# Performance work log

Hardware: AMD Instinct MI355X
Metric: run time of the kernel (lower is better)

## Reference

```python
import jax, jax.numpy as jnp
import numpy as np

B, H, W, C = 4, 128, 128, 192
NH, WS, SS = 6, 16, 8
N = WS * WS
HD = C // NH
SCALE = HD ** -0.5
CONV_SCALE = 0.01


def _win_part(x, ws):
    b, h, w, c = x.shape
    x = x.reshape(b, h // ws, ws, w // ws, ws, c).transpose(0, 1, 3, 2, 4, 5)
    return x.reshape(-1, ws * ws, c)


def _win_rev(win, ws, h, w):
    b = win.shape[0] // ((h // ws) * (w // ws))
    x = win.reshape(b, h // ws, w // ws, ws, ws, -1).transpose(0, 1, 3, 2, 4, 5)
    return x.reshape(b, h, w, -1)


def _ln(x, g, b):
    m = x.mean(-1, keepdims=True)
    v = x.var(-1, keepdims=True)
    return (x - m) * jax.lax.rsqrt(v + 1e-5) * g + b


def _conv3(x, w, b):
    return jax.lax.conv_general_dilated(x, w, (1, 1), 'SAME', dimension_numbers=('NHWC', 'HWIO', 'NHWC')) + b


def _rpi_sa(ws):
    coords = np.stack(np.meshgrid(np.arange(ws), np.arange(ws), indexing='ij'))
    cf = coords.reshape(2, -1)
    rc = (cf[:, :, None] - cf[:, None, :]).transpose(1, 2, 0).copy()
    rc[:, :, 0] += ws - 1
    rc[:, :, 1] += ws - 1
    rc[:, :, 0] *= 2 * ws - 1
    return rc.sum(-1)


def _attn_mask(h, w, ws, ss):
    img = np.zeros((1, h, w, 1), dtype=np.float32)
    slices = (slice(0, -ws), slice(-ws, -ss), slice(-ss, None))
    cnt = 0
    for hs in slices:
        for wsl in slices:
            img[:, hs, wsl, :] = cnt
            cnt += 1
    mw = img.reshape(1, h // ws, ws, w // ws, ws, 1).transpose(0, 1, 3, 2, 4, 5).reshape(-1, ws * ws)
    am = mw[:, None, :] - mw[:, :, None]
    return np.where(am != 0, -100.0, 0.0).astype(np.float32)


def setup_inputs() -> dict:
    key = jax.random.key(0)
    ks = jax.random.split(key, 10)
    std = 0.02
    return {
        'x': jax.random.normal(ks[0], (B, H * W, C), jnp.float32),
        'qkv_w': jax.random.normal(ks[1], (C, 3 * C), jnp.float32) * std,
        'qkv_b': jnp.zeros((3 * C,), jnp.float32),
        'proj_w': jax.random.normal(ks[2], (C, C), jnp.float32) * std,
        'proj_b': jnp.zeros((C,), jnp.float32),
        'rpb': jax.random.normal(ks[3], ((2 * WS - 1) ** 2, NH), jnp.float32) * std,
        'norm1_w': jnp.ones((C,), jnp.float32),
        'norm1_b': jnp.zeros((C,), jnp.float32),
        'norm2_w': jnp.ones((C,), jnp.float32),
        'norm2_b': jnp.zeros((C,), jnp.float32),
        'conv1_w': jax.random.normal(ks[4], (3, 3, C, C // 3), jnp.float32) * std,
        'conv1_b': jnp.zeros((C // 3,), jnp.float32),
        'conv2_w': jax.random.normal(ks[5], (3, 3, C // 3, C), jnp.float32) * std,
        'conv2_b': jnp.zeros((C,), jnp.float32),
        'ca1_w': jax.random.normal(ks[6], (C, C // 30), jnp.float32) * std,
        'ca1_b': jnp.zeros((C // 30,), jnp.float32),
        'ca2_w': jax.random.normal(ks[7], (C // 30, C), jnp.float32) * std,
        'ca2_b': jnp.zeros((C,), jnp.float32),
        'fc1_w': jax.random.normal(ks[8], (C, 4 * C), jnp.float32) * std,
        'fc1_b': jnp.zeros((4 * C,), jnp.float32),
        'fc2_w': jax.random.normal(ks[9], (4 * C, C), jnp.float32) * std,
        'fc2_b': jnp.zeros((C,), jnp.float32),
        'rpi': jnp.asarray(_rpi_sa(WS), jnp.int32),
        'attn_mask': jnp.asarray(_attn_mask(H, W, WS, SS)),
    }


def reference(x, qkv_w, qkv_b, proj_w, proj_b, rpb, norm1_w, norm1_b, norm2_w, norm2_b,
              conv1_w, conv1_b, conv2_w, conv2_b, ca1_w, ca1_b, ca2_w, ca2_b,
              fc1_w, fc1_b, fc2_w, fc2_b, rpi, attn_mask):
    b = x.shape[0]
    shortcut = x
    xn = _ln(x, norm1_w, norm1_b).reshape(b, H, W, C)

    # CAB conv branch: conv3x3 -> GELU -> conv3x3 -> channel attention
    cv = jax.nn.gelu(_conv3(xn, conv1_w, conv1_b), approximate=False)
    cv = _conv3(cv, conv2_w, conv2_b)
    pooled = cv.mean(axis=(1, 2))                                  # [b, C] global avg pool
    ca = jax.nn.sigmoid(jnp.maximum(pooled @ ca1_w + ca1_b, 0.0) @ ca2_w + ca2_b)
    conv_x = (cv * ca[:, None, None, :]).reshape(b, H * W, C)

    # shifted window attention
    shifted = jnp.roll(xn, (-SS, -SS), axis=(1, 2))
    xw = _win_part(shifted, WS)                                    # [b*nw, N, C]
    b_ = xw.shape[0]
    qkv = (xw @ qkv_w + qkv_b).reshape(b_, N, 3, NH, HD).transpose(2, 0, 3, 1, 4)
    q, k, v = qkv[0] * SCALE, qkv[1], qkv[2]                       # [b_, NH, N, HD]
    attn = jnp.einsum('whnd,whmd->whnm', q, k)                     # [b_, NH, N, N]
    bias = rpb[rpi.reshape(-1)].reshape(N, N, NH).transpose(2, 0, 1)
    attn = attn + bias[None]
    nw = attn_mask.shape[0]
    attn = attn.reshape(b, nw, NH, N, N) + attn_mask[None, :, None]
    attn = jax.nn.softmax(attn, axis=-1).reshape(b_, NH, N, N)
    out = jnp.einsum('whnm,whmd->whnd', attn, v).transpose(0, 2, 1, 3).reshape(b_, N, C)
    out = out @ proj_w + proj_b
    rev = _win_rev(out, WS, H, W)
    attn_x = jnp.roll(rev, (SS, SS), axis=(1, 2)).reshape(b, H * W, C)

    y = shortcut + attn_x + conv_x * CONV_SCALE

    # MLP
    yn = _ln(y, norm2_w, norm2_b)
    mlp = jax.nn.gelu(yn @ fc1_w + fc1_b, approximate=False) @ fc2_w + fc2_b
    return y + mlp
```

## Files before the change

kernel.cpp:

```cpp
#include <hip/hip_runtime.h>
#include <hip/hip_bf16.h>
#include <cstdint>
#include <cstddef>

#define BB 4
#define CC 192
#define NHEAD 6
#define WSZ 16
#define SSH 8
#define NTOK 256
#define HD 32
#define HWPIX 16384
#define TTOT 65536
#define WWID 128
#define SCALE_Q 0.17677669529663687f
#define CONV_SC 0.01f
#define PSTR 264
#define KSTR 40

typedef __hip_bfloat16 bf16;
typedef __attribute__((ext_vector_type(8))) short short8;
typedef __attribute__((ext_vector_type(4))) float float4v;

__device__ __forceinline__ float b2f(bf16 v) { return __bfloat162float(v); }
__device__ __forceinline__ bf16 f2b(float v) { return __float2bfloat16(v); }
__device__ __forceinline__ unsigned short f2bu(float f) {
  bf16 h = __float2bfloat16(f);
  return *reinterpret_cast<unsigned short*>(&h);
}
__device__ __forceinline__ float gelu_exact(float x) {
  return 0.5f * x * (1.0f + erff(x * 0.7071067811865475f));
}
__device__ __forceinline__ short8 ld8z(const bf16* p, bool ok) {
  if (ok) return *(const short8*)p;
  short8 z = {0, 0, 0, 0, 0, 0, 0, 0};
  return z;
}
__device__ __forceinline__ void glds16(const void* g, void* l) {
  __builtin_amdgcn_global_load_lds(
      (const __attribute__((address_space(1))) unsigned int*)g,
      (__attribute__((address_space(3))) unsigned int*)l, 16, 0, 0);
}

__global__ __launch_bounds__(256) void k_ln1(const float* __restrict__ x,
                                             const float* __restrict__ g,
                                             const float* __restrict__ b,
                                             bf16* __restrict__ xn) {
  int wv = threadIdx.x >> 6, lane = threadIdx.x & 63;
  int tok = blockIdx.x * 4 + wv;
  size_t row = (size_t)tok * CC;
  float v0 = x[row + lane], v1 = x[row + lane + 64], v2 = x[row + lane + 128];
  float s = v0 + v1 + v2, ss = v0 * v0 + v1 * v1 + v2 * v2;
#pragma unroll
  for (int off = 1; off < 64; off <<= 1) {
    s += __shfl_xor(s, off, 64);
    ss += __shfl_xor(ss, off, 64);
  }
  float mean = s * (1.0f / CC);
  float rstd = rsqrtf(ss * (1.0f / CC) - mean * mean + 1e-5f);
  xn[row + lane]       = f2b((v0 - mean) * rstd * g[lane]       + b[lane]);
  xn[row + lane + 64]  = f2b((v1 - mean) * rstd * g[lane + 64]  + b[lane + 64]);
  xn[row + lane + 128] = f2b((v2 - mean) * rstd * g[lane + 128] + b[lane + 128]);
}

__global__ __launch_bounds__(256) void k_biasq(const int* __restrict__ rpi,
                                               const float* __restrict__ rpb,
                                               float* __restrict__ biasQ) {
  int k = threadIdx.x;
  int h = blockIdx.x >> 8;
  int q = blockIdx.x & 255;
  biasQ[(size_t)blockIdx.x * 256 + ((k & 15) << 4) + (k >> 4)] =
      rpb[rpi[q * 256 + k] * NHEAD + h];
}

__global__ __launch_bounds__(256) void k_wprep(const float* __restrict__ c1w,
                                               const float* __restrict__ c2w,
                                               bf16* __restrict__ wT1,
                                               bf16* __restrict__ wT2) {
  int i = blockIdx.x * 256 + threadIdx.x;
  {
    int tap = i / (64 * 192); int r = i % (64 * 192);
    int oc = r / 192, ci = r % 192;
    wT1[i] = f2b(c1w[(size_t)(tap * 192 + ci) * 64 + oc]);
  }
  {
    int tap = i / (192 * 64); int r = i % (192 * 64);
    int oc = r / 64, ci = r % 64;
    wT2[i] = f2b(c2w[(size_t)(tap * 64 + ci) * 192 + oc]);
  }
}

__global__ __launch_bounds__(256) void k_wprep2(const float* __restrict__ fc1w,
                                                const float* __restrict__ fc2w,
                                                bf16* __restrict__ wF1,
                                                bf16* __restrict__ wF2) {
  int i = blockIdx.x * 256 + threadIdx.x;
  {
    int n = i / 192, k = i % 192;
    wF1[i] = f2b(fc1w[(size_t)k * 768 + n]);
  }
  {
    int n = i / 768, k = i % 768;
    wF2[i] = f2b(fc2w[(size_t)k * 192 + n]);
  }
}

__global__ __launch_bounds__(256) void k_wprep3(const float* __restrict__ qkvw,
                                                const float* __restrict__ projw,
                                                bf16* __restrict__ wQv,
                                                bf16* __restrict__ wP) {
  int i = blockIdx.x * 256 + threadIdx.x;
  if (i < 576 * 192) {
    int n = i / 192, k = i % 192;
    wQv[i] = f2b(qkvw[(size_t)k * 576 + n]);
  }
  if (i < 192 * 192) {
    int n = i / 192, k = i % 192;
    wP[i] = f2b(projw[(size_t)k * 192 + n]);
  }
}

__global__ __launch_bounds__(256, 2) void k_qkvws(const bf16* __restrict__ xn,
                                                  const bf16* __restrict__ wQv,
                                                  const float* __restrict__ qb,
                                                  bf16* __restrict__ Qg,
                                                  bf16* __restrict__ Kg,
                                                  bf16* __restrict__ Vg) {
  __shared__ unsigned short wl[192 * 192];
  int cg = blockIdx.x / 128, tb = blockIdx.x - cg * 128;
  int tid = threadIdx.x;
  int wave = tid >> 6, lane = tid & 63;
  int lm = lane & 15, lq = lane >> 4;

  const char* src = (const char*)wQv + (size_t)cg * 73728;
#pragma unroll
  for (int j = 0; j < 18; ++j) {
    int ci = j * 256 + tid;
    int r = ci / 24, c = ci - r * 24;
    glds16(src + (size_t)r * 384 + ((c ^ (r & 7)) << 4),
           (char*)wl + (size_t)(j * 256 + wave * 64) * 16);
  }
  __syncthreads();

  short8 wfr[3][6];
#pragma unroll
  for (int nt = 0; nt < 3; ++nt) {
    int rl = wave * 48 + nt * 16 + lm;
#pragma unroll
    for (int ks = 0; ks < 6; ++ks)
      wfr[nt][ks] = *(const short8*)&wl[rl * 192 + (((ks * 4 + lq) ^ (rl & 7)) << 3)];
  }
  float4 b4[3];
  int head[3], d0[3];
#pragma unroll
  for (int nt = 0; nt < 3; ++nt) {
    int n0p = wave * 48 + nt * 16 + lq * 4;
    b4[nt] = *(const float4*)(qb + cg * 192 + n0p);
    head[nt] = n0p >> 5;
    d0[nt] = n0p & 31;
  }
  bf16* dst = (cg == 0) ? Qg : (cg == 1) ? Kg : Vg;
  float scale = (cg == 0) ? SCALE_Q : 1.f;

  int tok0b = tb * 512;
#pragma unroll 2
  for (int t = 0; t < 32; ++t) {
    int tok0 = tok0b + t * 16;
    const bf16* arow = xn + (size_t)(tok0 + lm) * CC + lq * 8;
    int tg = tok0 + lm;
    int b = tg >> 14;
    int pix = tg & 16383;
    int gh = pix >> 7, gw = pix & 127;
    int hs = (gh + 120) & 127, wsx = (gw + 120) & 127;
    int wdx = (b << 6) + ((hs >> 4) << 3) + (wsx >> 4);
    int ndx = ((hs & 15) << 4) + (wsx & 15);
    size_t base = ((size_t)wdx * NHEAD) * NTOK * HD + (size_t)ndx * HD;

    float4v acc[3];
#pragma unroll
    for (int nt = 0; nt < 3; ++nt) acc[nt] = (float4v){0.f, 0.f, 0.f, 0.f};
#pragma unroll
    for (int ks = 0; ks < 6; ++ks) {
      short8 tf = *(const short8*)(arow + ks * 32);
#pragma unroll
      for (int nt = 0; nt < 3; ++nt)
        acc[nt] = __builtin_amdgcn_mfma_f32_16x16x32_bf16(wfr[nt][ks], tf, acc[nt], 0, 0, 0);
    }
#pragma unroll
    for (int nt = 0; nt < 3; ++nt) {
      unsigned short u0 = f2bu((acc[nt][0] + b4[nt].x) * scale);
      unsigned short u1 = f2bu((acc[nt][1] + b4[nt].y) * scale);
      unsigned short u2 = f2bu((acc[nt][2] + b4[nt].z) * scale);
      unsigned short u3 = f2bu((acc[nt][3] + b4[nt].w) * scale);
      uint2 pk;
      pk.x = (unsigned)u0 | ((unsigned)u1 << 16);
      pk.y = (unsigned)u2 | ((unsigned)u3 << 16);
      *(uint2*)(dst + base + (size_t)head[nt] * NTOK * HD + d0[nt]) = pk;
    }
  }
}

__global__ __launch_bounds__(256) void k_attn3(const bf16* __restrict__ Qg,
                                               const bf16* __restrict__ Kg,
                                               const bf16* __restrict__ Vg,
                                               const float* __restrict__ biasP,
                                               bf16* __restrict__ AO) {
  __shared__ unsigned short PTw[4][16 * PSTR];
  __shared__ unsigned short VT[32 * PSTR];
  __shared__ unsigned short KL[256 * KSTR];
  int wh = blockIdx.x >> 1, half = blockIdx.x & 1;
  int wdx = wh / NHEAD, h = wh - wdx * NHEAD;
  int wl = wdx & 63;
  int wr = wl >> 3, wc = wl & 7;
  int tid = threadIdx.x;
  int wave = tid >> 6, lane = tid & 63;
  int lm = lane & 15, lq = lane >> 4;
  int q0 = half * 128;
  bool needmask = (wr == 7) || (wc == 7);

  {
    const uint4* vp = (const uint4*)(Vg + ((size_t)wh * NTOK + tid) * HD);
    uint4 vv[4] = {vp[0], vp[1], vp[2], vp[3]};
    const uint4* kp = (const uint4*)(Kg + ((size_t)wh * NTOK + tid) * HD);
    uint4 kv[4] = {kp[0], kp[1], kp[2], kp[3]};
#pragma unroll
    for (int i = 0; i < 4; ++i) {
      unsigned arr[4] = {vv[i].x, vv[i].y, vv[i].z, vv[i].w};
#pragma unroll
      for (int j = 0; j < 4; ++j) {
        int d = i * 8 + j * 2;
        VT[d * PSTR + tid]       = (unsigned short)(arr[j] & 0xffffu);
        VT[(d + 1) * PSTR + tid] = (unsigned short)(arr[j] >> 16);
      }
      *(uint4*)&KL[tid * KSTR + i * 8] = kv[i];
    }
  }
  __syncthreads();

  int wsk = (wc << 4) + lm;
  int ridk_w = (wsk >= 112) + (wsk >= 120);
  unsigned short* PT = &PTw[wave][0];

  float4v oacc[2][2];
#pragma unroll
  for (int rt = 0; rt < 2; ++rt)
#pragma unroll
    for (int c2 = 0; c2 < 2; ++c2) oacc[rt][c2] = (float4v){0.f, 0.f, 0.f, 0.f};
  float linv[2][4];

#pragma unroll
  for (int rt = 0; rt < 2; ++rt) {
    int qrow = q0 + wave * 32 + rt * 16;
    short8 aq = *(const short8*)(Qg + ((size_t)wh * NTOK + qrow + lm) * HD + lq * 8);
    float4v sacc[16];
#pragma unroll
    for (int ct = 0; ct < 16; ++ct) sacc[ct] = (float4v){0.f, 0.f, 0.f, 0.f};
#pragma unroll
    for (int ct = 0; ct < 16; ++ct) {
      short8 kf = *(const short8*)&KL[(ct * 16 + lm) * KSTR + lq * 8];
      sacc[ct] = __builtin_amdgcn_mfma_f32_16x16x32_bf16(aq, kf, sacc[ct], 0, 0, 0);
    }
#pragma unroll
    for (int reg = 0; reg < 4; ++reg) {
      int nq = qrow + lq * 4 + reg;
      const float* bp = biasP + ((size_t)(h * 256 + nq)) * 256 + lm * 16;
      float bb[16];
      *(float4*)&bb[0]  = ((const float4*)bp)[0];
      *(float4*)&bb[4]  = ((const float4*)bp)[1];
      *(float4*)&bb[8]  = ((const float4*)bp)[2];
      *(float4*)&bb[12] = ((const float4*)bp)[3];
      float sv[16];
      float mx = -1.0e30f;
      if (needmask) {
        int hsq = (wr << 4) + (nq >> 4), wsq = (wc << 4) + (nq & 15);
        int ridq = ((hsq >= 112) + (hsq >= 120)) * 3 + ((wsq >= 112) + (wsq >= 120));
#pragma unroll
        for (int ct = 0; ct < 16; ++ct) {
          int hsk = (wr << 4) + ct;
          int ridk = ((hsk >= 112) + (hsk >= 120)) * 3 + ridk_w;
          float s = sacc[ct][reg] + bb[ct] + ((ridk != ridq) ? -100.f : 0.f);
          sv[ct] = s;
          mx = fmaxf(mx, s);
        }
      } else {
#pragma unroll
        for (int ct = 0; ct < 16; ++ct) {
          float s = sacc[ct][reg] + bb[ct];
          sv[ct] = s;
          mx = fmaxf(mx, s);
        }
      }
#pragma unroll
      for (int off = 1; off < 16; off <<= 1) mx = fmaxf(mx, __shfl_xor(mx, off, 64));
      float l = 0.f;
#pragma unroll
      for (int ct = 0; ct < 16; ++ct) {
        float p = __expf(sv[ct] - mx);
        l += p;
        PT[(lq * 4 + reg) * PSTR + ct * 16 + lm] = f2bu(p);
      }
#pragma unroll
      for (int off = 1; off < 16; off <<= 1) l += __shfl_xor(l, off, 64);
      linv[rt][reg] = 1.f / l;
    }
#pragma unroll
    for (int kb = 0; kb < 8; ++kb) {
      short8 pf = *(const short8*)&PT[lm * PSTR + kb * 32 + lq * 8];
#pragma unroll
      for (int c2 = 0; c2 < 2; ++c2) {
        short8 vf = *(const short8*)&VT[(c2 * 16 + lm) * PSTR + kb * 32 + lq * 8];
        oacc[rt][c2] = __builtin_amdgcn_mfma_f32_16x16x32_bf16(pf, vf, oacc[rt][c2], 0, 0, 0);
      }
    }
  }
#pragma unroll
  for (int rt = 0; rt < 2; ++rt)
#pragma unroll
    for (int c2 = 0; c2 < 2; ++c2) {
      int d = c2 * 16 + lm;
#pragma unroll
      for (int reg = 0; reg < 4; ++reg) {
        int nq = q0 + wave * 32 + rt * 16 + lq * 4 + reg;
        AO[((size_t)wdx * NTOK + nq) * CC + h * HD + d] =
            f2b(oacc[rt][c2][reg] * linv[rt][reg]);
      }
    }
}

__global__ __launch_bounds__(256, 2) void k_projws(const bf16* __restrict__ AO,
                                                   const bf16* __restrict__ wP,
                                                   const float* __restrict__ pb,
                                                   const float* __restrict__ x,
                                                   float* __restrict__ y) {
  __shared__ unsigned short wl[192 * 192];
  int tb = blockIdx.x;
  int tid = threadIdx.x;
  int wave = tid >> 6, lane = tid & 63;
  int lm = lane & 15, lq = lane >> 4;

  const char* src = (const char*)wP;
#pragma unroll
  for (int j = 0; j < 18; ++j) {
    int ci = j * 256 + tid;
    int r = ci / 24, c = ci - r * 24;
    glds16(src + (size_t)r * 384 + ((c ^ (r & 7)) << 4),
           (char*)wl + (size_t)(j * 256 + wave * 64) * 16);
  }
  __syncthreads();

  short8 wfr[3][6];
#pragma unroll
  for (int nt = 0; nt < 3; ++nt) {
    int rl = wave * 48 + nt * 16 + lm;
#pragma unroll
    for (int ks = 0; ks < 6; ++ks)
      wfr[nt][ks] = *(const short8*)&wl[rl * 192 + (((ks * 4 + lq) ^ (rl & 7)) << 3)];
  }
  float4 b4[3];
#pragma unroll
  for (int nt = 0; nt < 3; ++nt)
    b4[nt] = *(const float4*)(pb + wave * 48 + nt * 16 + lq * 4);

  int r0b = tb * 512;
#pragma unroll 2
  for (int t = 0; t < 32; ++t) {
    int r0 = r0b + t * 16;
    const bf16* arow = AO + (size_t)(r0 + lm) * CC + lq * 8;
    int r = r0 + lm;
    int wdx = r >> 8, n = r & 255;
    int wb = wdx >> 6, wlx = wdx & 63;
    int hs = ((wlx >> 3) << 4) + (n >> 4);
    int wsx = ((wlx & 7) << 4) + (n & 15);
    int gh = (hs + SSH) & 127, gw = (wsx + SSH) & 127;
    size_t drow = ((size_t)wb * HWPIX + (size_t)gh * WWID + gw) * CC;

    float4v acc[3];
#pragma unroll
    for (int nt = 0; nt < 3; ++nt) acc[nt] = (float4v){0.f, 0.f, 0.f, 0.f};
#pragma unroll
    for (int ks = 0; ks < 6; ++ks) {
      short8 tf = *(const short8*)(arow + ks * 32);
#pragma unroll
      for (int nt = 0; nt < 3; ++nt)
        acc[nt] = __builtin_amdgcn_mfma_f32_16x16x32_bf16(wfr[nt][ks], tf, acc[nt], 0, 0, 0);
    }
#pragma unroll
    for (int nt = 0; nt < 3; ++nt) {
      int col0 = wave * 48 + nt * 16 + lq * 4;
      float4 xv = *(const float4*)(x + drow + col0);
      float4 ov;
      ov.x = xv.x + acc[nt][0] + b4[nt].x;
      ov.y = xv.y + acc[nt][1] + b4[nt].y;
      ov.z = xv.z + acc[nt][2] + b4[nt].z;
      ov.w = xv.w + acc[nt][3] + b4[nt].w;
      *(float4*)(y + drow + col0) = ov;
    }
  }
}

__global__ __launch_bounds__(512, 1) void k_conv1l(const bf16* __restrict__ xn,
                                                   const bf16* __restrict__ wT1,
                                                   const float* __restrict__ c1b,
                                                   bf16* __restrict__ cv1) {
  __shared__ unsigned short xs[3 * 128 * 192];
  int hh = blockIdx.x & 127, b = blockIdx.x >> 7;
  int tid = threadIdx.x;
  int wave = tid >> 6, lane = tid & 63;
  int lm = lane & 15, lq = lane >> 4;
  int ph = wave >> 2;
  int oc = (wave & 3) * 16 + lm;

#pragma unroll
  for (int r = 0; r < 3; ++r) {
    int gh = hh + r - 1;
    if ((unsigned)gh < 128u) {
      const char* src = (const char*)(xn + (size_t)(b * HWPIX + gh * WWID) * CC);
#pragma unroll
      for (int j = 0; j < 6; ++j) {
        int c = j * 512 + tid;
        int px = c / 24, kc = c - px * 24;
        glds16(src + (size_t)px * 384 + ((size_t)(kc ^ (px & 7)) << 4),
               (char*)xs + ((size_t)(r * 3072 + j * 512 + wave * 64)) * 16);
      }
    }
  }
  __syncthreads();

  float4v acc[4];
#pragma unroll
  for (int t = 0; t < 4; ++t) acc[t] = (float4v){0.f, 0.f, 0.f, 0.f};

  short8 w[6], wn[6];
#pragma unroll
  for (int ks = 0; ks < 6; ++ks)
    w[ks] = *(const short8*)(wT1 + ((size_t)oc) * CC + ks * 32 + lq * 8);
#pragma unroll
  for (int tap = 0; tap < 9; ++tap) {
    if (tap < 8) {
#pragma unroll
      for (int ks = 0; ks < 6; ++ks)
        wn[ks] = *(const short8*)(wT1 + ((size_t)((tap + 1) * 64) + oc) * CC + ks * 32 + lq * 8);
    }
    int kh = tap / 3, kw = tap % 3;
    int gh = hh + kh - 1;
    if ((unsigned)gh < 128u) {
      const unsigned short* row = &xs[kh * 24576];
#pragma unroll
      for (int ks = 0; ks < 6; ++ks) {
#pragma unroll
        for (int t = 0; t < 4; ++t) {
          int px = ph * 64 + t * 16 + lm + kw - 1;
          int pxc = px < 0 ? 0 : (px > 127 ? 127 : px);
          short8 av = *(const short8*)&row[pxc * 192 + (((ks * 4 + lq) ^ (pxc & 7)) << 3)];
          short8 zz = {0, 0, 0, 0, 0, 0, 0, 0};
          short8 a = ((unsigned)px < 128u) ? av : zz;
          acc[t] = __builtin_amdgcn_mfma_f32_16x16x32_bf16(a, w[ks], acc[t], 0, 0, 0);
        }
      }
    }
#pragma unroll
    for (int ks = 0; ks < 6; ++ks) w[ks] = wn[ks];
  }
  float bias = c1b[oc];
#pragma unroll
  for (int t = 0; t < 4; ++t) {
    int pxb = ph * 64 + t * 16 + lq * 4;
    size_t base = ((size_t)b * HWPIX + (size_t)hh * WWID + pxb) * 64 + oc;
    cv1[base]       = f2b(gelu_exact(acc[t][0] + bias));
    cv1[base + 64]  = f2b(gelu_exact(acc[t][1] + bias));
    cv1[base + 128] = f2b(gelu_exact(acc[t][2] + bias));
    cv1[base + 192] = f2b(gelu_exact(acc[t][3] + bias));
  }
}

__global__ __launch_bounds__(512, 2) void k_conv2l(const bf16* __restrict__ cv1,
                                                   const bf16* __restrict__ wT2,
                                                   const float* __restrict__ c2b,
                                                   bf16* __restrict__ cv2) {
  __shared__ unsigned short cs[3 * 128 * 64];
  int hh = blockIdx.x & 127, b = blockIdx.x >> 7;
  int tid = threadIdx.x;
  int wave = tid >> 6, lane = tid & 63;
  int lm = lane & 15, lq = lane >> 4;
  int ph = wave >> 2;
  int og = wave & 3;

#pragma unroll
  for (int r = 0; r < 3; ++r) {
    int gh = hh + r - 1;
    if ((unsigned)gh < 128u) {
      const char* src = (const char*)(cv1 + (size_t)(b * HWPIX + gh * WWID) * 64);
#pragma unroll
      for (int j = 0; j < 2; ++j) {
        int c = j * 512 + tid;
        int px = c >> 3, kc = c & 7;
        glds16(src + (size_t)px * 128 + ((size_t)(kc ^ (px & 7)) << 4),
               (char*)cs + ((size_t)(r * 1024 + j * 512 + wave * 64)) * 16);
      }
    }
  }
  __syncthreads();

  float4v acc[3][4];
#pragma unroll
  for (int nt = 0; nt < 3; ++nt)
#pragma unroll
    for (int t = 0; t < 4; ++t) acc[nt][t] = (float4v){0.f, 0.f, 0.f, 0.f};

  short8 w[3][2], wn[3][2];
#pragma unroll
  for (int nt = 0; nt < 3; ++nt) {
    int oc = og * 48 + nt * 16 + lm;
#pragma unroll
    for (int ks = 0; ks < 2; ++ks)
      w[nt][ks] = *(const short8*)(wT2 + ((size_t)oc) * 64 + ks * 32 + lq * 8);
  }
#pragma unroll
  for (int tap = 0; tap < 9; ++tap) {
    if (tap < 8) {
#pragma unroll
      for (int nt = 0; nt < 3; ++nt) {
        int oc = og * 48 + nt * 16 + lm;
#pragma unroll
        for (int ks = 0; ks < 2; ++ks)
          wn[nt][ks] = *(const short8*)(wT2 + ((size_t)((tap + 1) * 192) + oc) * 64 + ks * 32 + lq * 8);
      }
    }
    int kh = tap / 3, kw = tap % 3;
    int gh = hh + kh - 1;
    if ((unsigned)gh < 128u) {
      const unsigned short* row = &cs[kh * 8192];
#pragma unroll
      for (int ks = 0; ks < 2; ++ks) {
#pragma unroll
        for (int t = 0; t < 4; ++t) {
          int px = ph * 64 + t * 16 + lm + kw - 1;
          int pxc = px < 0 ? 0 : (px > 127 ? 127 : px);
          short8 av = *(const short8*)&row[pxc * 64 + (((ks * 4 + lq) ^ (pxc & 7)) << 3)];
          short8 zz = {0, 0, 0, 0, 0, 0, 0, 0};
          short8 a = ((unsigned)px < 128u) ? av : zz;
#pragma unroll
          for (int nt = 0; nt < 3; ++nt)
            acc[nt][t] = __builtin_amdgcn_mfma_f32_16x16x32_bf16(a, w[nt][ks], acc[nt][t], 0, 0, 0);
        }
      }
    }
#pragma unroll
    for (int nt = 0; nt < 3; ++nt)
#pragma unroll
      for (int ks = 0; ks < 2; ++ks) w[nt][ks] = wn[nt][ks];
  }
#pragma unroll
  for (int nt = 0; nt < 3; ++nt) {
    int oc = og * 48 + nt * 16 + lm;
    float bias = c2b[oc];
#pragma unroll
    for (int t = 0; t < 4; ++t) {
      int pxb = ph * 64 + t * 16 + lq * 4;
      size_t base = ((size_t)b * HWPIX + (size_t)hh * WWID + pxb) * CC + oc;
      cv2[base]           = f2b(acc[nt][t][0] + bias);
      cv2[base + CC]      = f2b(acc[nt][t][1] + bias);
      cv2[base + 2 * CC]  = f2b(acc[nt][t][2] + bias);
      cv2[base + 3 * CC]  = f2b(acc[nt][t][3] + bias);
    }
  }
}

__global__ __launch_bounds__(192) void k_pool(const bf16* __restrict__ cv2,
                                              float* __restrict__ pooled) {
  int t = threadIdx.x;
  int b = blockIdx.x >> 7;
  int pc = blockIdx.x & 127;
  const bf16* base = cv2 + ((size_t)b * HWPIX + (size_t)pc * 128) * CC + t;
  float s = 0.f;
#pragma unroll 4
  for (int p = 0; p < 128; ++p) s += b2f(base[(size_t)p * CC]);
  atomicAdd(&pooled[b * CC + t], s);
}

__global__ __launch_bounds__(192) void k_ca(const float* __restrict__ pooled,
                                            const float* __restrict__ w1,
                                            const float* __restrict__ b1,
                                            const float* __restrict__ w2,
                                            const float* __restrict__ b2,
                                            float* __restrict__ ca) {
  __shared__ float pld[CC];
  __shared__ float t1[6];
  int t = threadIdx.x, b = blockIdx.x;
  pld[t] = pooled[b * CC + t] * (1.0f / HWPIX);
  __syncthreads();
  if (t < 6) {
    float s = b1[t];
    for (int c = 0; c < CC; ++c) s += pld[c] * w1[c * 6 + t];
    t1[t] = fmaxf(s, 0.f);
  }
  __syncthreads();
  float s = b2[t];
#pragma unroll
  for (int k = 0; k < 6; ++k) s += t1[k] * w2[k * CC + t];
  ca[b * CC + t] = 1.f / (1.f + __expf(-s));
}

__global__ __launch_bounds__(256) void k_ln2(const float* __restrict__ y,
                                             const bf16* __restrict__ cv2,
                                             const float* __restrict__ ca,
                                             const float* __restrict__ g2,
                                             const float* __restrict__ b2,
                                             bf16* __restrict__ yn) {
  int wv = threadIdx.x >> 6, lane = threadIdx.x & 63;
  int tok = blockIdx.x * 4 + wv;
  const float* cab = ca + (tok >> 14) * CC;
  size_t row = (size_t)tok * CC;
  float v0 = y[row + lane]       + b2f(cv2[row + lane])       * cab[lane]       * CONV_SC;
  float v1 = y[row + lane + 64]  + b2f(cv2[row + lane + 64])  * cab[lane + 64]  * CONV_SC;
  float v2 = y[row + lane + 128] + b2f(cv2[row + lane + 128]) * cab[lane + 128] * CONV_SC;
  float s = v0 + v1 + v2, ss = v0 * v0 + v1 * v1 + v2 * v2;
#pragma unroll
  for (int off = 1; off < 64; off <<= 1) {
    s += __shfl_xor(s, off, 64);
    ss += __shfl_xor(ss, off, 64);
  }
  float mean = s * (1.0f / CC);
  float rstd = rsqrtf(ss * (1.0f / CC) - mean * mean + 1e-5f);
  yn[row + lane]       = f2b((v0 - mean) * rstd * g2[lane]       + b2[lane]);
  yn[row + lane + 64]  = f2b((v1 - mean) * rstd * g2[lane + 64]  + b2[lane + 64]);
  yn[row + lane + 128] = f2b((v2 - mean) * rstd * g2[lane + 128] + b2[lane + 128]);
}

__global__ __launch_bounds__(256, 2) void k_fc1ws(const bf16* __restrict__ yn,
                                                  const bf16* __restrict__ wF1,
                                                  const float* __restrict__ fb1,
                                                  bf16* __restrict__ h) {
  __shared__ unsigned short wl[192 * 192];
  int cg = blockIdx.x & 3, tb = blockIdx.x >> 2;
  int tid = threadIdx.x;
  int wave = tid >> 6, lane = tid & 63;
  int lm = lane & 15, lq = lane >> 4;

  const char* src = (const char*)wF1 + (size_t)cg * 73728;
#pragma unroll
  for (int j = 0; j < 18; ++j) {
    int ci = j * 256 + tid;
    int r = ci / 24, c = ci - r * 24;
    glds16(src + (size_t)r * 384 + ((c ^ (r & 7)) << 4),
           (char*)wl + (size_t)(j * 256 + wave * 64) * 16);
  }
  __syncthreads();

  short8 wfr[3][6];
#pragma unroll
  for (int nt = 0; nt < 3; ++nt) {
    int rl = wave * 48 + nt * 16 + lm;
#pragma unroll
    for (int ks = 0; ks < 6; ++ks)
      wfr[nt][ks] = *(const short8*)&wl[rl * 192 + (((ks * 4 + lq) ^ (rl & 7)) << 3)];
  }
  float4 b4[3];
#pragma unroll
  for (int nt = 0; nt < 3; ++nt)
    b4[nt] = *(const float4*)(fb1 + cg * 192 + wave * 48 + nt * 16 + lq * 4);

  int tok0b = tb * 512;
#pragma unroll 2
  for (int t = 0; t < 32; ++t) {
    int tok0 = tok0b + t * 16;
    const bf16* arow = yn + (size_t)(tok0 + lm) * CC + lq * 8;
    float4v acc[3];
#pragma unroll
    for (int nt = 0; nt < 3; ++nt) acc[nt] = (float4v){0.f, 0.f, 0.f, 0.f};
#pragma unroll
    for (int ks = 0; ks < 6; ++ks) {
      short8 tf = *(const short8*)(arow + ks * 32);
#pragma unroll
      for (int nt = 0; nt < 3; ++nt)
        acc[nt] = __builtin_amdgcn_mfma_f32_16x16x32_bf16(wfr[nt][ks], tf, acc[nt], 0, 0, 0);
    }
    bf16* hrow = h + (size_t)(tok0 + lm) * 768 + cg * 192 + wave * 48 + lq * 4;
#pragma unroll
    for (int nt = 0; nt < 3; ++nt) {
      unsigned short u0 = f2bu(gelu_exact(acc[nt][0] + b4[nt].x));
      unsigned short u1 = f2bu(gelu_exact(acc[nt][1] + b4[nt].y));
      unsigned short u2 = f2bu(gelu_exact(acc[nt][2] + b4[nt].z));
      unsigned short u3 = f2bu(gelu_exact(acc[nt][3] + b4[nt].w));
      uint2 pk;
      pk.x = (unsigned)u0 | ((unsigned)u1 << 16);
      pk.y = (unsigned)u2 | ((unsigned)u3 << 16);
      *(uint2*)(hrow + nt * 16) = pk;
    }
  }
}

__global__ __launch_bounds__(256, 2) void k_fc2m(const bf16* __restrict__ h,
                                                 const bf16* __restrict__ wF2,
                                                 const float* __restrict__ fb2,
                                                 const float* __restrict__ y,
                                                 const bf16* __restrict__ cv2,
                                                 const float* __restrict__ ca,
                                                 float* __restrict__ out) {
  __shared__ unsigned short ha[2][4096];
  __shared__ unsigned short wbt[2][6144];
  int r0 = blockIdx.x * 128;
  int tid = threadIdx.x;
  int wave = tid >> 6, lane = tid & 63;
  int lm = lane & 15, lq = lane >> 4;

  const char* hsrc = (const char*)(h + (size_t)r0 * 768);
  const char* wsrc = (const char*)wF2;

  float4v acc[2][12];
#pragma unroll
  for (int mt = 0; mt < 2; ++mt)
#pragma unroll
    for (int nt = 0; nt < 12; ++nt) acc[mt][nt] = (float4v){0.f, 0.f, 0.f, 0.f};

  auto stage = [&](int kc, int b) {
    int k0b = kc * 64;
#pragma unroll
    for (int j = 0; j < 2; ++j) {
      int c = j * 256 + tid;
      glds16(hsrc + (size_t)(c >> 2) * 1536 + k0b + (c & 3) * 16,
             (char*)&ha[b][0] + (j * 256 + wave * 64) * 16);
    }
#pragma unroll
    for (int j = 0; j < 3; ++j) {
      int c = j * 256 + tid;
      glds16(wsrc + (size_t)(c >> 2) * 1536 + k0b + (c & 3) * 16,
             (char*)&wbt[b][0] + (j * 256 + wave * 64) * 16);
    }
  };

  stage(0, 0);
  __syncthreads();
#pragma unroll 1
  for (int kc = 0; kc < 24; ++kc) {
    int cur = kc & 1;
    if (kc < 23) stage(kc + 1, cur ^ 1);
    short8 af[2], bf[12];
#pragma unroll
    for (int mt = 0; mt < 2; ++mt)
      af[mt] = *(const short8*)&ha[cur][(wave * 32 + mt * 16 + lm) * 32 + lq * 8];
#pragma unroll
    for (int nt = 0; nt < 12; ++nt)
      bf[nt] = *(const short8*)&wbt[cur][(nt * 16 + lm) * 32 + lq * 8];
#pragma unroll
    for (int mt = 0; mt < 2; ++mt)
#pragma unroll
      for (int nt = 0; nt < 12; ++nt)
        acc[mt][nt] = __builtin_amdgcn_mfma_f32_16x16x32_bf16(af[mt], bf[nt], acc[mt][nt], 0, 0, 0);
    __syncthreads();
  }

  const float* cab = ca + (r0 >> 14) * CC;
#pragma unroll
  for (int nt = 0; nt < 12; ++nt) {
    int col = nt * 16 + lm;
    float bias = fb2[col];
    float cas = cab[col] * CONV_SC;
#pragma unroll
    for (int mt = 0; mt < 2; ++mt) {
#pragma unroll
      for (int reg = 0; reg < 4; ++reg) {
        int tok = r0 + wave * 32 + mt * 16 + lq * 4 + reg;
        size_t idx = (size_t)tok * CC + col;
        out[idx] = y[idx] + b2f(cv2[idx]) * cas + acc[mt][nt][reg] + bias;
      }
    }
  }
}

extern "C" void kernel_launch(void* const* d_in, const int* in_sizes, int n_in,
                              void* d_out, int out_size, void* d_ws, size_t ws_size,
                              hipStream_t stream) {
  const float* x      = (const float*)d_in[0];
  const float* qkv_w  = (const float*)d_in[1];
  const float* qkv_b  = (const float*)d_in[2];
  const float* proj_w = (const float*)d_in[3];
  const float* proj_b = (const float*)d_in[4];
  const float* rpb    = (const float*)d_in[5];
  const float* n1w    = (const float*)d_in[6];
  const float* n1b    = (const float*)d_in[7];
  const float* n2w    = (const float*)d_in[8];
  const float* n2b    = (const float*)d_in[9];
  const float* c1w    = (const float*)d_in[10];
  const float* c1b    = (const float*)d_in[11];
  const float* c2w    = (const float*)d_in[12];
  const float* c2b    = (const float*)d_in[13];
  const float* ca1w   = (const float*)d_in[14];
  const float* ca1b   = (const float*)d_in[15];
  const float* ca2w   = (const float*)d_in[16];
  const float* ca2b   = (const float*)d_in[17];
  const float* fc1w   = (const float*)d_in[18];
  const float* fc1b   = (const float*)d_in[19];
  const float* fc2w   = (const float*)d_in[20];
  const float* fc2b   = (const float*)d_in[21];
  const int*   rpi    = (const int*)d_in[22];
  (void)in_sizes; (void)n_in; (void)out_size; (void)ws_size;

  char* wsb = (char*)d_ws;
  bf16*  xn    = (bf16*)(wsb + 0);
  bf16*  yn    = (bf16*)(wsb + 0);
  float* biasQ = (float*)(wsb + 25165824);
  bf16*  Qg    = (bf16*)(wsb + 26738688);
  bf16*  Kg    = (bf16*)(wsb + 51904512);
  bf16*  Vg    = (bf16*)(wsb + 77070336);
  bf16*  AO    = (bf16*)(wsb + 102236160);
  bf16*  hbuf  = (bf16*)(wsb + 26738688);
  float* y     = (float*)(wsb + 127401984);
  bf16*  cv1   = (bf16*)(wsb + 177733632);
  bf16*  cv2   = (bf16*)(wsb + 186122240);
  float* pool  = (float*)(wsb + 211288064);
  float* cavec = (float*)(wsb + 211291136);
  bf16*  wT1   = (bf16*)(wsb + 211294208);
  bf16*  wT2   = (bf16*)(wsb + 211515392);
  bf16*  wF1   = (bf16*)(wsb + 211736576);
  bf16*  wF2   = (bf16*)(wsb + 212031488);
  bf16*  wQv   = (bf16*)(wsb + 212326400);
  bf16*  wP    = (bf16*)(wsb + 212547584);
  float* out   = (float*)d_out;

  k_ln1<<<TTOT / 4, 256, 0, stream>>>(x, n1w, n1b, xn);
  k_biasq<<<NHEAD * NTOK, 256, 0, stream>>>(rpi, rpb, biasQ);
  k_wprep<<<432, 256, 0, stream>>>(c1w, c2w, wT1, wT2);
  k_wprep2<<<576, 256, 0, stream>>>(fc1w, fc2w, wF1, wF2);
  k_wprep3<<<576, 256, 0, stream>>>(qkv_w, proj_w, wQv, wP);
  k_qkvws<<<384, 256, 0, stream>>>(xn, wQv, qkv_b, Qg, Kg, Vg);
  k_attn3<<<BB * 64 * NHEAD * 2, 256, 0, stream>>>(Qg, Kg, Vg, biasQ, AO);
  k_projws<<<128, 256, 0, stream>>>(AO, wP, proj_b, x, y);
  k_conv1l<<<BB * 128, 512, 0, stream>>>(xn, wT1, c1b, cv1);
  k_conv2l<<<BB * 128, 512, 0, stream>>>(cv1, wT2, c2b, cv2);
  hipMemsetAsync(pool, 0, BB * CC * sizeof(float), stream);
  k_pool<<<512, 192, 0, stream>>>(cv2, pool);
  k_ca<<<BB, 192, 0, stream>>>(pool, ca1w, ca1b, ca2w, ca2b, cavec);
  k_ln2<<<TTOT / 4, 256, 0, stream>>>(y, cv2, cavec, n2w, n2b, yn);
  k_fc1ws<<<512, 256, 0, stream>>>(yn, wF1, fc1b, hbuf);
  k_fc2m<<<512, 256, 0, stream>>>(hbuf, wF2, fc2b, y, cv2, cavec, out);
}
```

Before: 544.1 us.

## Merge attention halves into 512-thread blocks and use exp2 softmax

The attention kernel now covers a whole window-head per 512-thread block instead of splitting the queries across two 256-thread blocks. This halves the K/V loads and transposes into shared memory, and the K and V staging is split between the two thread halves. The softmax switches to exp2: log2(e) is folded into the Q scale, the bias table and the mask constant. Wave priority hints are placed around the MFMA loops, and the P-tile stride is padded to reduce LDS bank conflicts. The larger block uses more shared memory, which may lower occupancy.

```diff
diff --git a/kernel.cpp b/kernel.cpp
--- a/kernel.cpp
+++ b/kernel.cpp
@@ -14,8 +14,12 @@
 #define TTOT 65536
 #define WWID 128
 #define SCALE_Q 0.17677669529663687f
+#define SCALE_QL2 0.25503485f
+#define LOG2E 1.4426950408889634f
+#define MASKL2 -144.2695041f
 #define CONV_SC 0.01f
 #define PSTR 264
+#define PSTR2 268
 #define KSTR 40
 
 typedef __hip_bfloat16 bf16;
@@ -70,7 +74,7 @@
   int h = blockIdx.x >> 8;
   int q = blockIdx.x & 255;
   biasQ[(size_t)blockIdx.x * 256 + ((k & 15) << 4) + (k >> 4)] =
-      rpb[rpi[q * 256 + k] * NHEAD + h];
+      rpb[rpi[q * 256 + k] * NHEAD + h] * LOG2E;
 }
 
 __global__ __launch_bounds__(256) void k_wprep(const float* __restrict__ c1w,
@@ -160,7 +164,7 @@
     d0[nt] = n0p & 31;
   }
   bf16* dst = (cg == 0) ? Qg : (cg == 1) ? Kg : Vg;
-  float scale = (cg == 0) ? SCALE_Q : 1.f;
+  float scale = (cg == 0) ? SCALE_QL2 : 1.f;
 
   int tok0b = tb * 512;
 #pragma unroll 2
@@ -200,29 +204,26 @@
   }
 }
 
-__global__ __launch_bounds__(256) void k_attn3(const bf16* __restrict__ Qg,
+__global__ __launch_bounds__(512) void k_attn4(const bf16* __restrict__ Qg,
                                                const bf16* __restrict__ Kg,
                                                const bf16* __restrict__ Vg,
                                                const float* __restrict__ biasP,
                                                bf16* __restrict__ AO) {
-  __shared__ unsigned short PTw[4][16 * PSTR];
+  __shared__ unsigned short PTw[8][16 * PSTR2];
   __shared__ unsigned short VT[32 * PSTR];
   __shared__ unsigned short KL[256 * KSTR];
-  int wh = blockIdx.x >> 1, half = blockIdx.x & 1;
+  int wh = blockIdx.x;
   int wdx = wh / NHEAD, h = wh - wdx * NHEAD;
   int wl = wdx & 63;
   int wr = wl >> 3, wc = wl & 7;
   int tid = threadIdx.x;
   int wave = tid >> 6, lane = tid & 63;
   int lm = lane & 15, lq = lane >> 4;
-  int q0 = half * 128;
   bool needmask = (wr == 7) || (wc == 7);
 
-  {
+  if (tid < 256) {
     const uint4* vp = (const uint4*)(Vg + ((size_t)wh * NTOK + tid) * HD);
     uint4 vv[4] = {vp[0], vp[1], vp[2], vp[3]};
-    const uint4* kp = (const uint4*)(Kg + ((size_t)wh * NTOK + tid) * HD);
-    uint4 kv[4] = {kp[0], kp[1], kp[2], kp[3]};
 #pragma unroll
     for (int i = 0; i < 4; ++i) {
       unsigned arr[4] = {vv[i].x, vv[i].y, vv[i].z, vv[i].w};
@@ -232,8 +233,13 @@
         VT[d * PSTR + tid]       = (unsigned short)(arr[j] & 0xffffu);
         VT[(d + 1) * PSTR + tid] = (unsigned short)(arr[j] >> 16);
       }
-      *(uint4*)&KL[tid * KSTR + i * 8] = kv[i];
-    }
+    }
+  } else {
+    int key = tid - 256;
+    const uint4* kp = (const uint4*)(Kg + ((size_t)wh * NTOK + key) * HD);
+#pragma unroll
+    for (int i = 0; i < 4; ++i)
+      *(uint4*)&KL[key * KSTR + i * 8] = kp[i];
   }
   __syncthreads();
 
@@ -250,16 +256,18 @@
 
 #pragma unroll
   for (int rt = 0; rt < 2; ++rt) {
-    int qrow = q0 + wave * 32 + rt * 16;
+    int qrow = wave * 32 + rt * 16;
     short8 aq = *(const short8*)(Qg + ((size_t)wh * NTOK + qrow + lm) * HD + lq * 8);
     float4v sacc[16];
 #pragma unroll
     for (int ct = 0; ct < 16; ++ct) sacc[ct] = (float4v){0.f, 0.f, 0.f, 0.f};
+    __builtin_amdgcn_s_setprio(1);
 #pragma unroll
     for (int ct = 0; ct < 16; ++ct) {
       short8 kf = *(const short8*)&KL[(ct * 16 + lm) * KSTR + lq * 8];
       sacc[ct] = __builtin_amdgcn_mfma_f32_16x16x32_bf16(aq, kf, sacc[ct], 0, 0, 0);
     }
+    __builtin_amdgcn_s_setprio(0);
 #pragma unroll
     for (int reg = 0; reg < 4; ++reg) {
       int nq = qrow + lq * 4 + reg;
@@ -278,7 +286,7 @@
         for (int ct = 0; ct < 16; ++ct) {
           int hsk = (wr << 4) + ct;
           int ridk = ((hsk >= 112) + (hsk >= 120)) * 3 + ridk_w;
-          float s = sacc[ct][reg] + bb[ct] + ((ridk != ridq) ? -100.f : 0.f);
+          float s = sacc[ct][reg] + bb[ct] + ((ridk != ridq) ? MASKL2 : 0.f);
           sv[ct] = s;
           mx = fmaxf(mx, s);
         }
@@ -295,23 +303,25 @@
       float l = 0.f;
 #pragma unroll
       for (int ct = 0; ct < 16; ++ct) {
-        float p = __expf(sv[ct] - mx);
+        float p = __builtin_amdgcn_exp2f(sv[ct] - mx);
         l += p;
-        PT[(lq * 4 + reg) * PSTR + ct * 16 + lm] = f2bu(p);
+        PT[(lq * 4 + reg) * PSTR2 + ct * 16 + lm] = f2bu(p);
       }
 #pragma unroll
       for (int off = 1; off < 16; off <<= 1) l += __shfl_xor(l, off, 64);
       linv[rt][reg] = 1.f / l;
     }
+    __builtin_amdgcn_s_setprio(1);
 #pragma unroll
     for (int kb = 0; kb < 8; ++kb) {
-      short8 pf = *(const short8*)&PT[lm * PSTR + kb * 32 + lq * 8];
+      short8 pf = *(const short8*)&PT[lm * PSTR2 + kb * 32 + lq * 8];
 #pragma unroll
       for (int c2 = 0; c2 < 2; ++c2) {
         short8 vf = *(const short8*)&VT[(c2 * 16 + lm) * PSTR + kb * 32 + lq * 8];
         oacc[rt][c2] = __builtin_amdgcn_mfma_f32_16x16x32_bf16(pf, vf, oacc[rt][c2], 0, 0, 0);
       }
     }
+    __builtin_amdgcn_s_setprio(0);
   }
 #pragma unroll
   for (int rt = 0; rt < 2; ++rt)
@@ -320,7 +330,7 @@
       int d = c2 * 16 + lm;
 #pragma unroll
       for (int reg = 0; reg < 4; ++reg) {
-        int nq = q0 + wave * 32 + rt * 16 + lq * 4 + reg;
+        int nq = wave * 32 + rt * 16 + lq * 4 + reg;
         AO[((size_t)wdx * NTOK + nq) * CC + h * HD + d] =
             f2b(oacc[rt][c2][reg] * linv[rt][reg]);
       }
@@ -824,7 +834,7 @@
   k_wprep2<<<576, 256, 0, stream>>>(fc1w, fc2w, wF1, wF2);
   k_wprep3<<<576, 256, 0, stream>>>(qkv_w, proj_w, wQv, wP);
   k_qkvws<<<384, 256, 0, stream>>>(xn, wQv, qkv_b, Qg, Kg, Vg);
-  k_attn3<<<BB * 64 * NHEAD * 2, 256, 0, stream>>>(Qg, Kg, Vg, biasQ, AO);
+  k_attn4<<<BB * 64 * NHEAD, 512, 0, stream>>>(Qg, Kg, Vg, biasQ, AO);
   k_projws<<<128, 256, 0, stream>>>(AO, wP, proj_b, x, y);
   k_conv1l<<<BB * 128, 512, 0, stream>>>(xn, wT1, c1b, cv1);
   k_conv2l<<<BB * 128, 512, 0, stream>>>(cv1, wT2, c2b, cv2);
```

Result: slower. 557.6 us (+2.5%).
